# Kernel tuning notes

Hardware: AMD Instinct MI355X
Metric: run time of the kernel (lower is better)

## Reference

```python
import jax, jax.numpy as jnp
import numpy as np

N_MEL = 80; ARNN = 1024; ADIM = 128; EMB = 512; PRE = 256; DRNN = 1024; NF = 32; KS = 31
B = 32; NCTX = 512; T = 500
PAD = (KS - 1) // 2


def setup_inputs() -> dict:
    key = jax.random.key(0)
    ks = jax.random.split(key, 20)
    g = lambda k, shape: jax.random.normal(k, shape, dtype=jnp.float32) * 0.02
    return {
        "memory": jax.random.normal(ks[0], (B, NCTX, EMB), dtype=jnp.float32),
        "decoder_inputs": jax.random.normal(ks[1], (B, N_MEL, T), dtype=jnp.float32),
        "mask": jnp.zeros((B, NCTX), dtype=bool),
        "prenet_w1": g(ks[2], (PRE, N_MEL)),
        "prenet_w2": g(ks[3], (PRE, PRE)),
        "arnn_wih": g(ks[4], (4 * ARNN, PRE + EMB)),
        "arnn_whh": g(ks[5], (4 * ARNN, ARNN)),
        "arnn_bih": jnp.zeros((4 * ARNN,), jnp.float32),
        "arnn_bhh": jnp.zeros((4 * ARNN,), jnp.float32),
        "q_w": g(ks[6], (ADIM, ARNN)),
        "m_w": g(ks[7], (ADIM, EMB)),
        "loc_conv_w": g(ks[8], (NF, 2, KS)),
        "loc_w": g(ks[9], (ADIM, NF)),
        "v_w": g(ks[10], (ADIM,)),
        "drnn_wih": g(ks[11], (4 * DRNN, ARNN + EMB)),
        "drnn_whh": g(ks[12], (4 * DRNN, DRNN)),
        "drnn_bih": jnp.zeros((4 * DRNN,), jnp.float32),
        "drnn_bhh": jnp.zeros((4 * DRNN,), jnp.float32),
        "proj_w": g(ks[13], (N_MEL, DRNN + EMB)),
        "proj_b": jnp.zeros((N_MEL,), jnp.float32),
        "gate_w": g(ks[14], (1, DRNN + EMB)),
        "gate_b": jnp.zeros((1,), jnp.float32),
    }


def _lstm_cell(x, h, c, wih, whh, bih, bhh):
    # PyTorch LSTMCell gate order: i, f, g, o
    z = x @ wih.T + h @ whh.T + bih + bhh
    i, f, g, o = jnp.split(z, 4, axis=-1)
    c2 = jax.nn.sigmoid(f) * c + jax.nn.sigmoid(i) * jnp.tanh(g)
    h2 = jax.nn.sigmoid(o) * jnp.tanh(c2)
    return h2, c2


def reference(memory, decoder_inputs, mask,
              prenet_w1, prenet_w2,
              arnn_wih, arnn_whh, arnn_bih, arnn_bhh,
              q_w, m_w, loc_conv_w, loc_w, v_w,
              drnn_wih, drnn_whh, drnn_bih, drnn_bhh,
              proj_w, proj_b, gate_w, gate_b):
    b, n_ctx, emb = memory.shape
    n_mel, t_out = decoder_inputs.shape[1], decoder_inputs.shape[2]

    # (time, batch, n_mel) with a leading zero go-frame; PreNet (eval: no dropout)
    x = jnp.transpose(decoder_inputs, (2, 0, 1))
    x = jnp.concatenate([jnp.zeros((1, b, n_mel), x.dtype), x], axis=0)
    h = jax.nn.relu(x @ prenet_w1.T)
    h = jax.nn.relu(h @ prenet_w2.T)  # (T+1, B, PRE)
    inputs = h[:-1]  # T decoder steps

    proc_mem = memory @ m_w.T  # (B, n_ctx, ADIM)

    def step(carry, xin):
        ah, ac, dh, dc, aw, awc, actx = carry
        cell_in = jnp.concatenate([xin, actx], axis=-1)
        ah, ac = _lstm_cell(cell_in, ah, ac, arnn_wih, arnn_whh, arnn_bih, arnn_bhh)
        # location-sensitive attention
        aw_cat = jnp.stack([aw, awc], axis=1)  # (B, 2, n_ctx)
        loc = jax.lax.conv_general_dilated(
            aw_cat, loc_conv_w, window_strides=(1,), padding=[(PAD, PAD)],
            dimension_numbers=("NCH", "OIH", "NCH"))  # (B, NF, n_ctx)
        loc = jnp.transpose(loc, (0, 2, 1)) @ loc_w.T  # (B, n_ctx, ADIM)
        q = (ah @ q_w.T)[:, None, :]  # (B, 1, ADIM)
        e = jnp.tanh(q + proc_mem + loc) @ v_w  # (B, n_ctx)
        e = jnp.where(mask, -1e9, e)
        aw = jax.nn.softmax(e, axis=-1)
        actx = jnp.einsum("bn,bne->be", aw, memory)
        awc = awc + aw
        din = jnp.concatenate([ah, actx], axis=-1)
        dh, dc = _lstm_cell(din, dh, dc, drnn_wih, drnn_whh, drnn_bih, drnn_bhh)
        dhc = jnp.concatenate([dh, actx], axis=-1)
        mel = dhc @ proj_w.T + proj_b  # (B, n_mel)
        gate = dhc @ gate_w.T + gate_b  # (B, 1)
        return (ah, ac, dh, dc, aw, awc, actx), (mel, gate[:, 0])

    z32 = lambda *s: jnp.zeros(s, memory.dtype)
    carry0 = (z32(b, ARNN), z32(b, ARNN), z32(b, DRNN), z32(b, DRNN),
              z32(b, n_ctx), z32(b, n_ctx), z32(b, emb))
    _, (mels, gates) = jax.lax.scan(step, carry0, inputs)
    mel_out = jnp.transpose(mels, (1, 2, 0))   # (B, n_mel, T)
    gate_out = jnp.transpose(gates, (1, 0))    # (B, T)
    return mel_out, gate_out
```

## Files before the change

### kernel.cpp

```cpp
#include <hip/hip_runtime.h>

#define NBLK 256
#define NTHR 512

constexpr int kNMel = 80, kArnn = 1024, kAdim = 128, kEmb = 512, kPre = 256;
constexpr int kNF = 32, kKS = 31, kB = 32, kNctx = 512, kT = 500, kPad = 15;

constexpr int KT_A = 56;
constexpr int KT_D = 80;
constexpr int KT_ALL = KT_A + KT_D;

constexpr int OFF_PREB   = 0;
constexpr int OFF_PROCMB = OFF_PREB + kT * kB * kPre / 2;
constexpr int OFF_QWTB   = OFF_PROCMB + kB * kNctx * kAdim / 2;
constexpr int OFF_LWT    = OFF_QWTB + kAdim * kArnn / 2;
constexpr int OFF_STATE  = OFF_LWT + kAdim * 33;
constexpr int OFF_AHB    = OFF_STATE;
constexpr int OFF_DHB    = OFF_AHB + 2 * kB * kArnn / 2;
constexpr int OFF_DH     = OFF_DHB + 2 * kB * kArnn / 2;
constexpr int OFF_AC     = OFF_DH + 2 * kB * kArnn;
constexpr int OFF_DC     = OFF_AC + kB * kArnn;
constexpr int OFF_ACTX   = OFF_DC + kB * kArnn;
constexpr int OFF_AW     = OFF_ACTX + kB * kEmb;
constexpr int OFF_AWC    = OFF_AW + kB * kNctx;
constexpr int OFF_PAW    = OFF_AWC + kB * kNctx;
constexpr int OFF_NUM    = OFF_PAW + kB * kNctx;
constexpr int OFF_DEN    = OFF_NUM + 2 * kB * kEmb;
constexpr int OFF_END    = OFF_DEN + 2 * kB;
constexpr int STATE_SZ   = OFF_END - OFF_STATE;
constexpr int OFF_BAR    = OFF_END;
constexpr int BAR_LINES  = 266;
constexpr int OFF_PAN    = OFF_BAR + BAR_LINES * 32;
constexpr int PAN_SZ     = NBLK * KT_ALL * 256;
constexpr int OFF_GMB    = OFF_PAN + PAN_SZ;
constexpr int GMB_SZ     = kB * kNctx * kEmb / 2;

typedef __attribute__((ext_vector_type(4))) float fvec4;
typedef __attribute__((ext_vector_type(8))) short bh8_t;
typedef unsigned long long u64;
typedef unsigned short ushortt;

union U64u { u64 u; float2 f2; ushortt s[4]; };

constexpr int AH_O = 0;
constexpr int DH_O = 16384;
constexpr int AX_O = 32768;

union SMem {
  struct { ushortt stage[49152]; } x1;
  struct { float zra[4][2][64][4]; float zrd[4][2][64][4];
           float hb[2][32][4]; } x2;
  struct { float ahb_s[kArnn]; float vw_s[kAdim]; float psum[512]; float q_s[kAdim];
           float aw_s[96]; float awc_s[96]; float cw[kNF * 2 * kKS];
           float loc_s[64 * 33]; float p_s[64]; float lwt[kAdim * 33];
           float dhc[kArnn + kEmb]; float pprj[126];
           ushortt pm[64 * kAdim]; } b;
  struct { float x8[8][80]; float h1[8][256]; } p;
  struct { float mem_s[4][512]; } m;
};

__device__ __forceinline__ float sigf(float x) { return 1.0f / (1.0f + __expf(-x)); }
__device__ __forceinline__ float tanhfast(float x) { return 1.0f - 2.0f / (__expf(2.0f * x) + 1.0f); }

__device__ __forceinline__ ushortt bf16rn(float f) {
  unsigned u = __float_as_uint(f);
  unsigned r = (u + 0x7FFFu + ((u >> 16) & 1u)) >> 16;
  return (ushortt)r;
}
__device__ __forceinline__ float bf2f(ushortt v) {
  return __uint_as_float((unsigned)v << 16);
}

__device__ __forceinline__ u64 ald64(const void* p) {
  return __hip_atomic_load((const u64*)p, __ATOMIC_RELAXED, __HIP_MEMORY_SCOPE_AGENT);
}
__device__ __forceinline__ float alf(const float* p) {
  return __hip_atomic_load(p, __ATOMIC_RELAXED, __HIP_MEMORY_SCOPE_AGENT);
}
__device__ __forceinline__ void asf(float* p, float v) {
  __hip_atomic_store(p, v, __ATOMIC_RELAXED, __HIP_MEMORY_SCOPE_AGENT);
}
__device__ __forceinline__ void as64(void* p, u64 v) {
  __hip_atomic_store((u64*)p, v, __ATOMIC_RELAXED, __HIP_MEMORY_SCOPE_AGENT);
}
__device__ __forceinline__ unsigned alu(const unsigned* p) {
  return __hip_atomic_load(p, __ATOMIC_RELAXED, __HIP_MEMORY_SCOPE_AGENT);
}
__device__ __forceinline__ void asu(unsigned* p, unsigned v) {
  __hip_atomic_store(p, v, __ATOMIC_RELAXED, __HIP_MEMORY_SCOPE_AGENT);
}

__device__ __forceinline__ void gbar_full(unsigned* cnt, unsigned* gen, unsigned& genv) {
  __syncthreads();
  if (threadIdx.x == 0) {
    __threadfence();
    unsigned arrived = __hip_atomic_fetch_add(cnt, 1u, __ATOMIC_ACQ_REL, __HIP_MEMORY_SCOPE_AGENT) + 1u;
    if (arrived == (unsigned)NBLK) {
      __hip_atomic_store(cnt, 0u, __ATOMIC_RELAXED, __HIP_MEMORY_SCOPE_AGENT);
      __hip_atomic_fetch_add(gen, 1u, __ATOMIC_ACQ_REL, __HIP_MEMORY_SCOPE_AGENT);
    } else {
      while (__hip_atomic_load(gen, __ATOMIC_ACQUIRE, __HIP_MEMORY_SCOPE_AGENT) == genv) {
        __builtin_amdgcn_s_sleep(2);
      }
    }
    ++genv;
  }
  __syncthreads();
}

__device__ __forceinline__ void gbar_light(unsigned* bar, unsigned target, int bk, int tid) {
  asm volatile("s_waitcnt vmcnt(0) lgkmcnt(0)" ::: "memory");
  __syncthreads();
  if (bk == 0) {
    if (tid < 64) {
      if (tid == 0) asm volatile("s_waitcnt vmcnt(0)" ::: "memory");
      unsigned i0 = (unsigned)tid * 4, i1 = i0 + 1, i2 = i0 + 2, i3 = i0 + 3;
      for (;;) {
        bool ok = true;
        if (i0 != 0) ok = ok && (alu(&bar[i0 * 32]) >= target);
        ok = ok && (alu(&bar[i1 * 32]) >= target);
        ok = ok && (alu(&bar[i2 * 32]) >= target);
        ok = ok && (alu(&bar[i3 * 32]) >= target);
        if (__all(ok)) break;
        __builtin_amdgcn_s_sleep(1);
      }
      if (tid < 8) asu(&bar[(256 + tid) * 32], target);
    }
  } else {
    if (tid == 0) {
      asm volatile("s_waitcnt vmcnt(0)" ::: "memory");
      asu(&bar[bk * 32], target);
      unsigned* wk = &bar[(256 + (bk & 7)) * 32];
      while (alu(wk) < target) __builtin_amdgcn_s_sleep(1);
    }
  }
  __syncthreads();
}

__device__ __forceinline__ void stage_half1(int tid, const ushortt* __restrict__ AHBq,
    const ushortt* __restrict__ DHBp, const float* __restrict__ numq,
    const float* __restrict__ invden, ushortt* __restrict__ lds)
{
  const int uc = tid & 127;
  const int r0 = tid >> 7;
  const int chunk = uc >> 4, u8c = uc & 15;
  u64 va[8], vd[8], ax[8];
  #pragma unroll
  for (int i = 0; i < 8; ++i) {
    int row = r0 + 4 * i;
    va[i] = ald64(AHBq + (size_t)row * 1024 + uc * 4);
    vd[i] = ald64(DHBp + (size_t)row * 1024 + uc * 4);
  }
  #pragma unroll
  for (int i = 0; i < 8; ++i) {
    int row = r0 + 4 * i;
    const float* np = numq + (size_t)row * 512 + uc * 4;
    U64u a, b; a.u = ald64(np); b.u = ald64(np + 2);
    float s = invden[row];
    U64u pk;
    pk.s[0] = bf16rn(a.f2.x * s);  pk.s[1] = bf16rn(a.f2.y * s);
    pk.s[2] = bf16rn(b.f2.x * s);  pk.s[3] = bf16rn(b.f2.y * s);
    ax[i] = pk.u;
  }
  #pragma unroll
  for (int i = 0; i < 8; ++i) {
    int row = r0 + 4 * i;
    int sw = u8c ^ ((row & 7) << 1);
    int off = chunk * 2048 + row * 64 + sw * 4;
    *reinterpret_cast<u64*>(lds + AH_O + off) = va[i];
    *reinterpret_cast<u64*>(lds + DH_O + off) = vd[i];
    *reinterpret_cast<u64*>(lds + AX_O + off) = ax[i];
  }
}
__device__ __forceinline__ void load_half2(int tid, const ushortt* __restrict__ AHBq,
    const ushortt* __restrict__ DHBp, u64* va, u64* vd)
{
  const int uc = tid & 127, r0 = tid >> 7;
  #pragma unroll
  for (int i = 0; i < 8; ++i) {
    int row = r0 + 4 * i;
    va[i] = ald64(AHBq + (size_t)row * 1024 + 512 + uc * 4);
    vd[i] = ald64(DHBp + (size_t)row * 1024 + 512 + uc * 4);
  }
}
__device__ __forceinline__ void write_half2(int tid, const u64* va, const u64* vd,
                                            ushortt* __restrict__ lds)
{
  const int uc = tid & 127, r0 = tid >> 7;
  const int chunk = uc >> 4, u8c = uc & 15;
  #pragma unroll
  for (int i = 0; i < 8; ++i) {
    int row = r0 + 4 * i;
    int sw = u8c ^ ((row & 7) << 1);
    int off = chunk * 2048 + row * 64 + sw * 4;
    *reinterpret_cast<u64*>(lds + AH_O + off) = va[i];
    *reinterpret_cast<u64*>(lds + DH_O + off) = vd[i];
  }
}

__device__ constexpr int lds_base(int LS, int kt) {
  if (LS == 0) {
    if (kt < 24) return AX_O + ((kt - 8) >> 1) * 2048;
    if (kt < 40) return AH_O + ((kt - 24) >> 1) * 2048;
    return AH_O + ((kt - 40) >> 1) * 2048;
  } else {
    if (kt < 16) return AH_O + (kt >> 1) * 2048;
    if (kt < 32) return AH_O + ((kt - 16) >> 1) * 2048;
    if (kt < 48) return AX_O + ((kt - 32) >> 1) * 2048;
    if (kt < 64) return DH_O + ((kt - 48) >> 1) * 2048;
    return DH_O + ((kt - 64) >> 1) * 2048;
  }
}

template<int LS, int W, int HALF>
__device__ __forceinline__ void consume(const ushortt* __restrict__ lds,
    const short* __restrict__ pan, const ushortt* __restrict__ preb_t,
    int l, fvec4& z0, fvec4& z1)
{
  const int m = l & 15, kg = l >> 4;
  bh8_t fA[4], fB[4], fC[4];
  auto ld4 = [&](int kt0, bh8_t* f) {
    #pragma unroll
    for (int i = 0; i < 4; ++i)
      f[i] = *reinterpret_cast<const bh8_t*>(pan + (size_t)(kt0 + i) * 512 + l * 8);
  };
  auto run4 = [&](int kt0, bh8_t* f) {
    #pragma unroll
    for (int i = 0; i < 4; ++i) {
      const int kt = kt0 + i;
      const int base = lds_base(LS, kt);
      const int sw = (2 * ((kt & 1) * 4 + kg)) ^ ((m & 7) << 1);
      bh8_t a0 = *reinterpret_cast<const bh8_t*>(lds + base + m * 64 + sw * 4);
      bh8_t a1 = *reinterpret_cast<const bh8_t*>(lds + base + (16 + m) * 64 + sw * 4);
      z0 = __builtin_amdgcn_mfma_f32_16x16x32_bf16(a0, f[i], z0, 0, 0, 0);
      z1 = __builtin_amdgcn_mfma_f32_16x16x32_bf16(a1, f[i], z1, 0, 0, 0);
    }
  };
  if constexpr (LS == 0 && HALF == 0) {
    ld4(8 + 4 * W, fA); ld4(24 + 4 * W, fB);
    run4(8 + 4 * W, fA); run4(24 + 4 * W, fB);
  } else if constexpr (LS == 0 && HALF == 1) {
    bh8_t p0[2], p1[2], pf[2];
    #pragma unroll
    for (int i = 0; i < 2; ++i) {
      const int kt = 2 * W + i;
      p0[i] = *reinterpret_cast<const bh8_t*>(preb_t + (size_t)m * 256 + kt * 32 + kg * 8);
      p1[i] = *reinterpret_cast<const bh8_t*>(preb_t + (size_t)(16 + m) * 256 + kt * 32 + kg * 8);
      pf[i] = *reinterpret_cast<const bh8_t*>(pan + (size_t)kt * 512 + l * 8);
    }
    ld4(40 + 4 * W, fA);
    #pragma unroll
    for (int i = 0; i < 2; ++i) {
      z0 = __builtin_amdgcn_mfma_f32_16x16x32_bf16(p0[i], pf[i], z0, 0, 0, 0);
      z1 = __builtin_amdgcn_mfma_f32_16x16x32_bf16(p1[i], pf[i], z1, 0, 0, 0);
    }
    run4(40 + 4 * W, fA);
  } else if constexpr (LS == 1 && HALF == 0) {
    ld4(4 * W, fA); ld4(32 + 4 * W, fB); ld4(48 + 4 * W, fC);
    run4(4 * W, fA); run4(32 + 4 * W, fB); run4(48 + 4 * W, fC);
  } else {
    ld4(16 + 4 * W, fA); ld4(64 + 4 * W, fB);
    run4(16 + 4 * W, fA); run4(64 + 4 * W, fB);
  }
}

extern "C" __global__ void __launch_bounds__(NTHR, 1)
decoder_kernel(const float* __restrict__ gmem, const float* __restrict__ dec,
               const unsigned char* __restrict__ mask,
               const float* __restrict__ pw1, const float* __restrict__ pw2,
               const float* __restrict__ awih, const float* __restrict__ awhh,
               const float* __restrict__ abih, const float* __restrict__ abhh,
               const float* __restrict__ qw, const float* __restrict__ mw,
               const float* __restrict__ cvw, const float* __restrict__ locw,
               const float* __restrict__ vw,
               const float* __restrict__ dwih, const float* __restrict__ dwhh,
               const float* __restrict__ dbih, const float* __restrict__ dbhh,
               const float* __restrict__ pjw, const float* __restrict__ pjb,
               const float* __restrict__ gw, const float* __restrict__ gb,
               float* __restrict__ out, float* __restrict__ ws, int useg)
{
  __shared__ SMem sm;
  __shared__ float s_invden[32];
  const int bk = blockIdx.x, tid = threadIdx.x;
  unsigned genv_f = 0, bcnt = 0;
  unsigned* bar = reinterpret_cast<unsigned*>(ws + OFF_BAR);
  unsigned* cntF = &bar[264 * 32];
  unsigned* genF = &bar[265 * 32];

  ushortt* PREBu = reinterpret_cast<ushortt*>(ws + OFF_PREB);
  ushortt* PROCMBu = reinterpret_cast<ushortt*>(ws + OFF_PROCMB);
  ushortt* QWTBu = reinterpret_cast<ushortt*>(ws + OFF_QWTB);
  float* LWT = ws + OFF_LWT;
  ushortt* AHBu = reinterpret_cast<ushortt*>(ws + OFF_AHB);
  ushortt* DHBu = reinterpret_cast<ushortt*>(ws + OFF_DHB);
  float* DH = ws + OFF_DH;
  float* AC = ws + OFF_AC;
  float* DC = ws + OFF_DC;
  float* ACTX = ws + OFF_ACTX;
  float* AWp = ws + OFF_AW;
  float* AWC = ws + OFF_AWC;
  float* PAW = ws + OFF_PAW;
  float* NUM = ws + OFF_NUM;
  float* DEN = ws + OFF_DEN;
  short* PANS = reinterpret_cast<short*>(ws + OFF_PAN);
  ushortt* GMB = reinterpret_cast<ushortt*>(ws + OFF_GMB);

  for (int i = bk * NTHR + tid; i < STATE_SZ; i += NBLK * NTHR) (ws + OFF_STATE)[i] = 0.f;
  for (int i = bk * NTHR + tid; i < kAdim * kArnn; i += NBLK * NTHR)
    QWTBu[i] = bf16rn(qw[i]);
  for (int i = bk * NTHR + tid; i < kAdim * kNF; i += NBLK * NTHR) {
    int d = i >> 5, f = i & 31;
    LWT[d * 33 + f] = locw[i];
  }
  gbar_full(cntF, genF, genv_f);

  if (bk == 0 && tid < 2 * kB) asf(&DEN[tid], 1.0f);
  for (int it = 0; it < 16; ++it) {
    int task0 = bk * 64 + it * 4;
    for (int i = tid; i < 2048; i += NTHR) {
      int pr = i >> 9, h = i & 511;
      sm.m.mem_s[pr][h] = gmem[(size_t)(task0 + pr) * kEmb + h];
    }
    __syncthreads();
    {
      int pr = tid >> 7, d = tid & 127;
      const float* mwr = mw + d * kEmb;
      float acc = 0.f;
      for (int h = 0; h < kEmb; ++h) acc = fmaf(sm.m.mem_s[pr][h], mwr[h], acc);
      PROCMBu[(size_t)(task0 + pr) * kAdim + d] = bf16rn(acc);
    }
    if (useg) {
      for (int i = tid; i < 2048; i += NTHR) {
        int pr = i >> 9, h = i & 511;
        GMB[(size_t)(task0 + pr) * kEmb + h] = bf16rn(sm.m.mem_s[pr][h]);
      }
    }
    __syncthreads();
  }
  for (int g = bk; g < 2000; g += NBLK) {
    int t_idx = g >> 2;
    int b0 = (g & 3) * 8;
    if (t_idx == 0) {
      for (int i = tid; i < 8 * kPre; i += NTHR)
        PREBu[(size_t)(b0 + (i >> 8)) * kPre + (i & 255)] = 0;
      continue;
    }
    for (int i = tid; i < 640; i += NTHR) {
      int bb = i / 80, m2 = i % 80;
      sm.p.x8[bb][m2] = dec[((size_t)(b0 + bb) * kNMel + m2) * kT + (t_idx - 1)];
    }
    __syncthreads();
    {
      int u = tid & 255, rep = tid >> 8;
      float acc[4] = {0.f, 0.f, 0.f, 0.f};
      for (int m2 = 0; m2 < 80; ++m2) {
        float w = pw1[u * kNMel + m2];
        #pragma unroll
        for (int r = 0; r < 4; ++r) acc[r] = fmaf(w, sm.p.x8[rep * 4 + r][m2], acc[r]);
      }
      #pragma unroll
      for (int r = 0; r < 4; ++r) sm.p.h1[rep * 4 + r][u] = fmaxf(acc[r], 0.f);
    }
    __syncthreads();
    {
      int u = tid & 255, rep = tid >> 8;
      float acc[4] = {0.f, 0.f, 0.f, 0.f};
      for (int k = 0; k < kPre; ++k) {
        float w = pw2[u * kPre + k];
        #pragma unroll
        for (int r = 0; r < 4; ++r) acc[r] = fmaf(w, sm.p.h1[rep * 4 + r][k], acc[r]);
      }
      #pragma unroll
      for (int r = 0; r < 4; ++r)
        PREBu[((size_t)t_idx * kB + b0 + rep * 4 + r) * kPre + u] = bf16rn(fmaxf(acc[r], 0.f));
    }
    __syncthreads();
  }
  {
    const int UNITS = NBLK * KT_ALL * 64;
    for (int u = bk * NTHR + tid; u < UNITS; u += NBLK * NTHR) {
      int bkk = u / (KT_ALL * 64);
      int rem = u - bkk * (KT_ALL * 64);
      int kta = rem >> 6, l = rem & 63;
      int lstm = (kta >= KT_A);
      int kt = lstm ? kta - KT_A : kta;
      int n = l & 15, kg = l >> 4;
      int r = (n >> 2) * 1024 + bkk * 4 + (n & 3);
      bh8_t v;
      #pragma unroll
      for (int j = 0; j < 8; ++j) {
        int k = kt * 32 + kg * 8 + j;
        float wv;
        if (!lstm) wv = (k < 768) ? awih[(size_t)r * 768 + k] : awhh[(size_t)r * 1024 + (k - 768)];
        else       wv = (k < 1536) ? dwih[(size_t)r * 1536 + k] : dwhh[(size_t)r * 1024 + (k - 1536)];
        v[j] = (short)bf16rn(wv);
      }
      *reinterpret_cast<bh8_t*>(PANS + (size_t)u * 8) = v;
    }
  }
  gbar_full(cntF, genF, genv_f);

  for (int t = 0; t <= kT; ++t) {
    const int p = t & 1, q = p ^ 1;
    float* nump = NUM + p * kB * kEmb;
    const float* numq = NUM + q * kB * kEmb;
    const ushortt* AHBq_ = AHBu + q * kB * kArnn;
    const ushortt* DHBp_ = DHBu + p * kB * kArnn;

    if (tid < kB) s_invden[tid] = 1.0f / alf(DEN + q * kB + tid);
    __syncthreads();
    if (t > 0 && tid < 64) {
      int idx = bk * 64 + tid;
      int b2 = idx >> 9;
      float invd = s_invden[b2];
      float av = PAW[idx] * invd;
      asf(&AWp[idx], av);
      asf(&AWC[idx], alf(&AWC[idx]) + av);
      asf(&ACTX[idx], alf(&numq[idx]) * invd);
    }
    if (t < kT) {
      if (tid < 64) asf(&nump[bk * 64 + tid], 0.f);
      if (bk == 0 && tid < kB) asf(DEN + p * kB + tid, 0.f);
    }
    {
      ushortt* XL = reinterpret_cast<ushortt*>(&sm);
      stage_half1(tid, AHBq_, DHBp_, numq, s_invden, XL);
      u64 vA2[8], vD2[8];
      load_half2(tid, AHBq_, DHBp_, vA2, vD2);
      __syncthreads();
      const int w8 = tid >> 6, l = tid & 63;
      fvec4 z0 = {0.f, 0.f, 0.f, 0.f}, z1 = z0;
      const ushortt* preb_t = PREBu + (size_t)t * kB * kPre;
      const short* panb = PANS + (size_t)bk * (KT_ALL * 512);
      const short* pand = panb + KT_A * 512;
      const bool aA = (w8 < 4) && (t < kT);
      const bool aD = (w8 >= 4) && (t > 0);
      if (aA) {
        switch (w8) {
          case 0: consume<0, 0, 0>(XL, panb, preb_t, l, z0, z1); break;
          case 1: consume<0, 1, 0>(XL, panb, preb_t, l, z0, z1); break;
          case 2: consume<0, 2, 0>(XL, panb, preb_t, l, z0, z1); break;
          default: consume<0, 3, 0>(XL, panb, preb_t, l, z0, z1); break;
        }
      } else if (aD) {
        switch (w8) {
          case 4: consume<1, 0, 0>(XL, pand, preb_t, l, z0, z1); break;
          case 5: consume<1, 1, 0>(XL, pand, preb_t, l, z0, z1); break;
          case 6: consume<1, 2, 0>(XL, pand, preb_t, l, z0, z1); break;
          default: consume<1, 3, 0>(XL, pand, preb_t, l, z0, z1); break;
        }
      }
      __syncthreads();
      write_half2(tid, vA2, vD2, XL);
      __syncthreads();
      if (aA) {
        switch (w8) {
          case 0: consume<0, 0, 1>(XL, panb, preb_t, l, z0, z1); break;
          case 1: consume<0, 1, 1>(XL, panb, preb_t, l, z0, z1); break;
          case 2: consume<0, 2, 1>(XL, panb, preb_t, l, z0, z1); break;
          default: consume<0, 3, 1>(XL, panb, preb_t, l, z0, z1); break;
        }
      } else if (aD) {
        switch (w8) {
          case 4: consume<1, 0, 1>(XL, pand, preb_t, l, z0, z1); break;
          case 5: consume<1, 1, 1>(XL, pand, preb_t, l, z0, z1); break;
          case 6: consume<1, 2, 1>(XL, pand, preb_t, l, z0, z1); break;
          default: consume<1, 3, 1>(XL, pand, preb_t, l, z0, z1); break;
        }
      }
      __syncthreads();
      if (w8 < 4) {
        *reinterpret_cast<fvec4*>(&sm.x2.zra[w8][0][l][0]) = z0;
        *reinterpret_cast<fvec4*>(&sm.x2.zra[w8][1][l][0]) = z1;
      } else {
        *reinterpret_cast<fvec4*>(&sm.x2.zrd[w8 - 4][0][l][0]) = z0;
        *reinterpret_cast<fvec4*>(&sm.x2.zrd[w8 - 4][1][l][0]) = z1;
      }
    }
    __syncthreads();
    if (tid < 256) {
      const int ls = tid >> 7, uu = (tid >> 5) & 3, b = tid & 31;
      const bool go = (ls == 0) ? (t < kT) : (t > 0);
      if (go) {
        const int mt = b >> 4, mm = b & 15;
        const int lane_base = (mm >> 2) * 16, rr = mm & 3;
        float zg[4];
        #pragma unroll
        for (int g = 0; g < 4; ++g) {
          int ln = lane_base + g * 4 + uu;
          float s;
          if (ls == 0)
            s = sm.x2.zra[0][mt][ln][rr] + sm.x2.zra[1][mt][ln][rr]
              + sm.x2.zra[2][mt][ln][rr] + sm.x2.zra[3][mt][ln][rr];
          else
            s = sm.x2.zrd[0][mt][ln][rr] + sm.x2.zrd[1][mt][ln][rr]
              + sm.x2.zrd[2][mt][ln][rr] + sm.x2.zrd[3][mt][ln][rr];
          int rg = g * 1024 + bk * 4 + uu;
          s += (ls ? dbih[rg] + dbhh[rg] : abih[rg] + abhh[rg]);
          zg[g] = s;
        }
        float* cst = ls ? DC : AC;
        const int idx = b * kArnn + bk * 4 + uu;
        float c = sigf(zg[1]) * cst[idx] + sigf(zg[0]) * tanhfast(zg[2]);
        cst[idx] = c;
        float h = sigf(zg[3]) * tanhfast(c);
        if (ls) asf(&DH[q * kB * kArnn + idx], h);
        sm.x2.hb[ls][b][uu] = h;
      }
    }
    __syncthreads();
    if (tid < 64) {
      int ls = tid >> 5, b = tid & 31;
      bool go2 = ls ? (t > 0) : (t < kT);
      if (go2) {
        U64u pk;
        #pragma unroll
        for (int j = 0; j < 4; ++j) pk.s[j] = bf16rn(sm.x2.hb[ls][b][j]);
        ushortt* dst = (ls ? (DHBu + q * kB * kArnn) : (AHBu + p * kB * kArnn)) + b * kArnn + bk * 4;
        as64(dst, pk.u);
      }
    }
    gbar_light(bar, ++bcnt, bk, tid);

    if (t < kT) {
      const int b = bk >> 3, sub = bk & 7, j0 = sub * 64;
      const int pbase = (sub == 0) ? 0 : 21 + (sub - 1) * 20;
      const int pcnt = (sub == 0) ? 21 : 20;
      const ushortt* AHBp_ = AHBu + p * kB * kArnn;
      if (tid < 256) {
        U64u v; v.u = ald64(AHBp_ + b * kArnn + tid * 4);
        #pragma unroll
        for (int j = 0; j < 4; ++j) sm.b.ahb_s[tid * 4 + j] = bf2f(v.s[j]);
      }
      for (int i = tid; i < 94; i += NTHR) {
        int jj = j0 - kPad + i;
        bool ok = (jj >= 0 && jj < kNctx);
        sm.b.aw_s[i] = ok ? alf(&AWp[b * kNctx + jj]) : 0.f;
        sm.b.awc_s[i] = ok ? alf(&AWC[b * kNctx + jj]) : 0.f;
      }
      for (int i = tid; i < kNF * 2 * kKS; i += NTHR) sm.b.cw[i] = cvw[i];
      for (int i = tid; i < kAdim * 33; i += NTHR) sm.b.lwt[i] = LWT[i];
      for (int i = tid; i < kAdim; i += NTHR) sm.b.vw_s[i] = vw[i];
      {
        const fvec4* src = reinterpret_cast<const fvec4*>(PROCMBu + (size_t)(b * kNctx + j0) * kAdim);
        fvec4* dst = reinterpret_cast<fvec4*>(sm.b.pm);
        for (int i = tid; i < 1024; i += NTHR) dst[i] = src[i];
      }
      if (sub < 4 && t > 0) {
        for (int i = tid; i < kArnn + kEmb; i += NTHR)
          sm.b.dhc[i] = (i < kArnn) ? alf(&DH[q * kB * kArnn + b * kArnn + i])
                                    : alf(&ACTX[b * kEmb + (i - kArnn)]);
      }
      __syncthreads();
      {
        int d = tid & 127, qr = tid >> 7;
        const ushortt* wq = QWTBu + (size_t)d * kArnn + qr * 256;
        const float* ahs = sm.b.ahb_s + qr * 256;
        float acc = 0.f;
        #pragma unroll 4
        for (int h8 = 0; h8 < 32; ++h8) {
          U64u a, c2;
          a.u = *reinterpret_cast<const u64*>(wq + h8 * 8);
          c2.u = *reinterpret_cast<const u64*>(wq + h8 * 8 + 4);
          #pragma unroll
          for (int j = 0; j < 4; ++j) acc = fmaf(bf2f(a.s[j]), ahs[h8 * 8 + j], acc);
          #pragma unroll
          for (int j = 0; j < 4; ++j) acc = fmaf(bf2f(c2.s[j]), ahs[h8 * 8 + 4 + j], acc);
        }
        sm.b.psum[tid] = acc;
      }
      __syncthreads();
      if (tid < kAdim)
        sm.b.q_s[tid] = sm.b.psum[tid] + sm.b.psum[128 + tid]
                      + sm.b.psum[256 + tid] + sm.b.psum[384 + tid];
      {
        int j = tid >> 3, f0 = (tid & 7) * 4;
        #pragma unroll
        for (int fi = 0; fi < 4; ++fi) {
          int f = f0 + fi;
          const float* w0 = &sm.b.cw[f * 62];
          float s = 0.f;
          for (int k = 0; k < kKS; ++k)
            s = fmaf(sm.b.aw_s[j + k], w0[k], fmaf(sm.b.awc_s[j + k], w0[31 + k], s));
          sm.b.loc_s[j * 33 + f] = s;
        }
      }
      if (sub < 4 && t > 0 && tid < pcnt * 6) {
        int ol = tid / 6, kc = tid % 6, og = pbase + ol;
        const float* row = (og < kNMel) ? pjw + (size_t)og * (kArnn + kEmb) : gw;
        const float* x = sm.b.dhc + kc * 256;
        const float* r2 = row + kc * 256;
        float acc = 0.f;
        for (int k = 0; k < 256; ++k) acc = fmaf(r2[k], x[k], acc);
        sm.b.pprj[tid] = acc;
      }
      __syncthreads();
      {
        int j = tid >> 3, grp = tid & 7, jj = j0 + j;
        float pe = 0.f;
        #pragma unroll 4
        for (int dd = 0; dd < 16; ++dd) {
          int d = grp + 8 * dd;
          float l2 = 0.f;
          const float* ls2 = &sm.b.loc_s[j * 33];
          const float* lw2 = &sm.b.lwt[d * 33];
          #pragma unroll 8
          for (int f = 0; f < kNF; ++f) l2 = fmaf(ls2[f], lw2[f], l2);
          float x = sm.b.q_s[d] + bf2f(sm.b.pm[j * kAdim + d]) + l2;
          pe = fmaf(sm.b.vw_s[d], tanhfast(x), pe);
        }
        pe += __shfl_xor(pe, 1);
        pe += __shfl_xor(pe, 2);
        pe += __shfl_xor(pe, 4);
        if (grp == 0) {
          float pv = mask[b * kNctx + jj] ? 0.f : __expf(pe);
          sm.b.p_s[j] = pv;
          PAW[b * kNctx + jj] = pv;
        }
      }
      if (sub < 4 && t > 0 && tid < pcnt) {
        int og = pbase + tid;
        float val = (og < kNMel) ? pjb[og] : gb[0];
        #pragma unroll
        for (int kc = 0; kc < 6; ++kc) val += sm.b.pprj[tid * 6 + kc];
        if (og < kNMel) out[((size_t)b * kNMel + og) * kT + (t - 1)] = val;
        else out[(size_t)kB * kNMel * kT + b * kT + (t - 1)] = val;
      }
      __syncthreads();
      if (tid < 64) {
        float v = sm.b.p_s[tid];
        #pragma unroll
        for (int o = 1; o < 64; o <<= 1) v += __shfl_xor(v, o);
        if (tid == 0) atomicAdd(DEN + p * kB + b, v);
      }
      if (useg) {
        const ushortt* memb = GMB + (size_t)(b * kNctx + j0) * kEmb + tid;
        float a0 = 0.f, a1 = 0.f, a2 = 0.f, a3 = 0.f;
        #pragma unroll 4
        for (int jj2 = 0; jj2 < 64; jj2 += 4) {
          a0 = fmaf(sm.b.p_s[jj2],     bf2f(memb[(size_t)jj2 * kEmb]), a0);
          a1 = fmaf(sm.b.p_s[jj2 + 1], bf2f(memb[(size_t)(jj2 + 1) * kEmb]), a1);
          a2 = fmaf(sm.b.p_s[jj2 + 2], bf2f(memb[(size_t)(jj2 + 2) * kEmb]), a2);
          a3 = fmaf(sm.b.p_s[jj2 + 3], bf2f(memb[(size_t)(jj2 + 3) * kEmb]), a3);
        }
        atomicAdd(&nump[b * kEmb + tid], (a0 + a1) + (a2 + a3));
      } else {
        const float* memb = gmem + (size_t)(b * kNctx + j0) * kEmb + tid;
        float a0 = 0.f, a1 = 0.f;
        #pragma unroll 8
        for (int jj2 = 0; jj2 < 64; jj2 += 2) {
          a0 = fmaf(sm.b.p_s[jj2], memb[(size_t)jj2 * kEmb], a0);
          a1 = fmaf(sm.b.p_s[jj2 + 1], memb[(size_t)(jj2 + 1) * kEmb], a1);
        }
        atomicAdd(&nump[b * kEmb + tid], a0 + a1);
      }
      gbar_light(bar, ++bcnt, bk, tid);
    }
  }

  if (bk < kB) {
    const int b = bk;
    for (int i = tid; i < kArnn + kEmb; i += NTHR)
      sm.b.dhc[i] = (i < kArnn) ? alf(&DH[1 * kB * kArnn + b * kArnn + i])
                                : alf(&ACTX[b * kEmb + (i - kArnn)]);
    __syncthreads();
    if (tid < 486) {
      int ol = tid / 6, kc = tid % 6;
      const float* row = (ol < kNMel) ? pjw + (size_t)ol * (kArnn + kEmb) : gw;
      const float* x = sm.b.dhc + kc * 256;
      const float* r2 = row + kc * 256;
      float acc = 0.f;
      for (int k = 0; k < 256; ++k) acc = fmaf(r2[k], x[k], acc);
      sm.b.psum[tid] = acc;
    }
    __syncthreads();
    if (tid < 81) {
      float val = (tid < kNMel) ? pjb[tid] : gb[0];
      #pragma unroll
      for (int kc = 0; kc < 6; ++kc) val += sm.b.psum[tid * 6 + kc];
      if (tid < kNMel) out[((size_t)b * kNMel + tid) * kT + (kT - 1)] = val;
      else out[(size_t)kB * kNMel * kT + b * kT + (kT - 1)] = val;
    }
  }
}

extern "C" void kernel_launch(void* const* d_in, const int* in_sizes, int n_in,
                              void* d_out, int out_size, void* d_ws, size_t ws_size,
                              hipStream_t stream) {
  const float* gmem = (const float*)d_in[0];
  const float* dec = (const float*)d_in[1];
  const unsigned char* mask = (const unsigned char*)d_in[2];
  const float* pw1 = (const float*)d_in[3];
  const float* pw2 = (const float*)d_in[4];
  const float* awih = (const float*)d_in[5];
  const float* awhh = (const float*)d_in[6];
  const float* abih = (const float*)d_in[7];
  const float* abhh = (const float*)d_in[8];
  const float* qw = (const float*)d_in[9];
  const float* mw = (const float*)d_in[10];
  const float* cvw = (const float*)d_in[11];
  const float* locw = (const float*)d_in[12];
  const float* vw = (const float*)d_in[13];
  const float* dwih = (const float*)d_in[14];
  const float* dwhh = (const float*)d_in[15];
  const float* dbih = (const float*)d_in[16];
  const float* dbhh = (const float*)d_in[17];
  const float* pjw = (const float*)d_in[18];
  const float* pjb = (const float*)d_in[19];
  const float* gw = (const float*)d_in[20];
  const float* gb = (const float*)d_in[21];
  float* out = (float*)d_out;
  float* ws = (float*)d_ws;

  int useg = (ws_size >= (size_t)(OFF_GMB + GMB_SZ) * sizeof(float)) ? 1 : 0;

  hipMemsetAsync((char*)d_ws + (size_t)OFF_BAR * sizeof(float), 0,
                 (size_t)BAR_LINES * 128, stream);
  hipLaunchKernelGGL(decoder_kernel, dim3(NBLK), dim3(NTHR), 0, stream,
                     gmem, dec, mask, pw1, pw2, awih, awhh, abih, abhh, qw, mw,
                     cvw, locw, vw, dwih, dwhh, dbih, dbhh, pjw, pjb, gw, gb,
                     out, ws, useg);
}
```

Baseline: 39.91 ms.

## Concentrate LSTM gate GEMMs on 64 blocks with per-wave full-K tiles

The LSTM gate matmuls were split over all 256 blocks, each handling 4 hidden units, with the K dimension split across waves and reduced through LDS. Now only 64 blocks do the LSTM work, each owning 16 hidden units. Each wave computes a full-K 16x16 tile for both LSTMs and does its own gate math, so the cross-wave partial-sum reduction goes away. The remaining 192 blocks sit idle during this phase. Each active block streams four times as many weight panels per step, which puts the LSTM phase's global load bandwidth on fewer CUs.

```diff
diff --git a/kernel.cpp b/kernel.cpp
--- a/kernel.cpp
+++ b/kernel.cpp
@@ -2,6 +2,7 @@
 
 #define NBLK 256
 #define NTHR 512
+#define NLB 64
 
 constexpr int kNMel = 80, kArnn = 1024, kAdim = 128, kEmb = 512, kPre = 256;
 constexpr int kNF = 32, kKS = 31, kB = 32, kNctx = 512, kT = 500, kPad = 15;
@@ -31,7 +32,7 @@
 constexpr int OFF_BAR    = OFF_END;
 constexpr int BAR_LINES  = 266;
 constexpr int OFF_PAN    = OFF_BAR + BAR_LINES * 32;
-constexpr int PAN_SZ     = NBLK * KT_ALL * 256;
+constexpr int PAN_SZ     = NLB * 4 * KT_ALL * 256;
 constexpr int OFF_GMB    = OFF_PAN + PAN_SZ;
 constexpr int GMB_SZ     = kB * kNctx * kEmb / 2;
 
@@ -47,9 +48,9 @@
 constexpr int AX_O = 32768;
 
 union SMem {
-  struct { ushortt stage[49152]; } x1;
-  struct { float zra[4][2][64][4]; float zrd[4][2][64][4];
-           float hb[2][32][4]; } x2;
+  struct { ushortt stage[49152];
+           float zs[8][2][64][4];
+           float hb[2][32][16]; } x1;
   struct { float ahb_s[kArnn]; float vw_s[kAdim]; float psum[512]; float q_s[kAdim];
            float aw_s[96]; float awc_s[96]; float cw[kNF * 2 * kKS];
            float loc_s[64 * 33]; float p_s[64]; float lwt[kAdim * 33];
@@ -212,55 +213,27 @@
   }
 }
 
-template<int LS, int W, int HALF>
-__device__ __forceinline__ void consume(const ushortt* __restrict__ lds,
-    const short* __restrict__ pan, const ushortt* __restrict__ preb_t,
-    int l, fvec4& z0, fvec4& z1)
+template<int LS, int HALF>
+__device__ __forceinline__ void lstm_half(const ushortt* __restrict__ lds,
+    const short* __restrict__ panw, const ushortt* __restrict__ preb_t,
+    int row, int m, int kg, int l, fvec4& z)
 {
-  const int m = l & 15, kg = l >> 4;
-  bh8_t fA[4], fB[4], fC[4];
-  auto ld4 = [&](int kt0, bh8_t* f) {
-    #pragma unroll
-    for (int i = 0; i < 4; ++i)
-      f[i] = *reinterpret_cast<const bh8_t*>(pan + (size_t)(kt0 + i) * 512 + l * 8);
-  };
-  auto run4 = [&](int kt0, bh8_t* f) {
-    #pragma unroll
-    for (int i = 0; i < 4; ++i) {
-      const int kt = kt0 + i;
+  constexpr int N = (LS == 0) ? (HALF == 0 ? 32 : 24) : (HALF == 0 ? 48 : 32);
+  #pragma unroll
+  for (int i = 0; i < N; ++i) {
+    int kt;
+    if (LS == 0) kt = (HALF == 0) ? (8 + i) : (i < 8 ? i : 32 + i);
+    else         kt = (HALF == 0) ? (i < 16 ? i : i + 16) : (i < 16 ? 16 + i : 48 + i);
+    bh8_t f = *reinterpret_cast<const bh8_t*>(panw + (size_t)((LS ? KT_A : 0) + kt) * 512 + l * 8);
+    bh8_t a;
+    if (LS == 0 && kt < 8) {
+      a = *reinterpret_cast<const bh8_t*>(preb_t + (size_t)row * kPre + kt * 32 + kg * 8);
+    } else {
       const int base = lds_base(LS, kt);
       const int sw = (2 * ((kt & 1) * 4 + kg)) ^ ((m & 7) << 1);
-      bh8_t a0 = *reinterpret_cast<const bh8_t*>(lds + base + m * 64 + sw * 4);
-      bh8_t a1 = *reinterpret_cast<const bh8_t*>(lds + base + (16 + m) * 64 + sw * 4);
-      z0 = __builtin_amdgcn_mfma_f32_16x16x32_bf16(a0, f[i], z0, 0, 0, 0);
-      z1 = __builtin_amdgcn_mfma_f32_16x16x32_bf16(a1, f[i], z1, 0, 0, 0);
-    }
-  };
-  if constexpr (LS == 0 && HALF == 0) {
-    ld4(8 + 4 * W, fA); ld4(24 + 4 * W, fB);
-    run4(8 + 4 * W, fA); run4(24 + 4 * W, fB);
-  } else if constexpr (LS == 0 && HALF == 1) {
-    bh8_t p0[2], p1[2], pf[2];
-    #pragma unroll
-    for (int i = 0; i < 2; ++i) {
-      const int kt = 2 * W + i;
-      p0[i] = *reinterpret_cast<const bh8_t*>(preb_t + (size_t)m * 256 + kt * 32 + kg * 8);
-      p1[i] = *reinterpret_cast<const bh8_t*>(preb_t + (size_t)(16 + m) * 256 + kt * 32 + kg * 8);
-      pf[i] = *reinterpret_cast<const bh8_t*>(pan + (size_t)kt * 512 + l * 8);
-    }
-    ld4(40 + 4 * W, fA);
-    #pragma unroll
-    for (int i = 0; i < 2; ++i) {
-      z0 = __builtin_amdgcn_mfma_f32_16x16x32_bf16(p0[i], pf[i], z0, 0, 0, 0);
-      z1 = __builtin_amdgcn_mfma_f32_16x16x32_bf16(p1[i], pf[i], z1, 0, 0, 0);
-    }
-    run4(40 + 4 * W, fA);
-  } else if constexpr (LS == 1 && HALF == 0) {
-    ld4(4 * W, fA); ld4(32 + 4 * W, fB); ld4(48 + 4 * W, fC);
-    run4(4 * W, fA); run4(32 + 4 * W, fB); run4(48 + 4 * W, fC);
-  } else {
-    ld4(16 + 4 * W, fA); ld4(64 + 4 * W, fB);
-    run4(16 + 4 * W, fA); run4(64 + 4 * W, fB);
+      a = *reinterpret_cast<const bh8_t*>(lds + base + row * 64 + sw * 4);
+    }
+    z = __builtin_amdgcn_mfma_f32_16x16x32_bf16(a, f, z, 0, 0, 0);
   }
 }
 
@@ -377,15 +350,17 @@
     __syncthreads();
   }
   {
-    const int UNITS = NBLK * KT_ALL * 64;
+    const int UNITS = NLB * 4 * KT_ALL * 64;
     for (int u = bk * NTHR + tid; u < UNITS; u += NBLK * NTHR) {
-      int bkk = u / (KT_ALL * 64);
-      int rem = u - bkk * (KT_ALL * 64);
+      int lb = u / (4 * KT_ALL * 64);
+      int rem = u - lb * (4 * KT_ALL * 64);
+      int nt = rem / (KT_ALL * 64);
+      rem -= nt * (KT_ALL * 64);
       int kta = rem >> 6, l = rem & 63;
       int lstm = (kta >= KT_A);
       int kt = lstm ? kta - KT_A : kta;
       int n = l & 15, kg = l >> 4;
-      int r = (n >> 2) * 1024 + bkk * 4 + (n & 3);
+      int r = (n >> 2) * 1024 + lb * 16 + nt * 4 + (n & 3);
       bh8_t v;
       #pragma unroll
       for (int j = 0; j < 8; ++j) {
@@ -422,102 +397,71 @@
       if (tid < 64) asf(&nump[bk * 64 + tid], 0.f);
       if (bk == 0 && tid < kB) asf(DEN + p * kB + tid, 0.f);
     }
-    {
+    if (bk < NLB) {
       ushortt* XL = reinterpret_cast<ushortt*>(&sm);
       stage_half1(tid, AHBq_, DHBp_, numq, s_invden, XL);
       u64 vA2[8], vD2[8];
       load_half2(tid, AHBq_, DHBp_, vA2, vD2);
       __syncthreads();
       const int w8 = tid >> 6, l = tid & 63;
-      fvec4 z0 = {0.f, 0.f, 0.f, 0.f}, z1 = z0;
+      const int nt = w8 & 3, mh = w8 >> 2;
+      const int m = l & 15, kg = l >> 4, row = mh * 16 + m;
+      fvec4 za = {0.f, 0.f, 0.f, 0.f}, zd = za;
       const ushortt* preb_t = PREBu + (size_t)t * kB * kPre;
-      const short* panb = PANS + (size_t)bk * (KT_ALL * 512);
-      const short* pand = panb + KT_A * 512;
-      const bool aA = (w8 < 4) && (t < kT);
-      const bool aD = (w8 >= 4) && (t > 0);
-      if (aA) {
-        switch (w8) {
-          case 0: consume<0, 0, 0>(XL, panb, preb_t, l, z0, z1); break;
-          case 1: consume<0, 1, 0>(XL, panb, preb_t, l, z0, z1); break;
-          case 2: consume<0, 2, 0>(XL, panb, preb_t, l, z0, z1); break;
-          default: consume<0, 3, 0>(XL, panb, preb_t, l, z0, z1); break;
-        }
-      } else if (aD) {
-        switch (w8) {
-          case 4: consume<1, 0, 0>(XL, pand, preb_t, l, z0, z1); break;
-          case 5: consume<1, 1, 0>(XL, pand, preb_t, l, z0, z1); break;
-          case 6: consume<1, 2, 0>(XL, pand, preb_t, l, z0, z1); break;
-          default: consume<1, 3, 0>(XL, pand, preb_t, l, z0, z1); break;
-        }
-      }
+      const short* panw = PANS + (size_t)(bk * 4 + nt) * KT_ALL * 512;
+      if (t < kT) lstm_half<0, 0>(XL, panw, preb_t, row, m, kg, l, za);
+      if (t > 0)  lstm_half<1, 0>(XL, panw, preb_t, row, m, kg, l, zd);
       __syncthreads();
       write_half2(tid, vA2, vD2, XL);
       __syncthreads();
-      if (aA) {
-        switch (w8) {
-          case 0: consume<0, 0, 1>(XL, panb, preb_t, l, z0, z1); break;
-          case 1: consume<0, 1, 1>(XL, panb, preb_t, l, z0, z1); break;
-          case 2: consume<0, 2, 1>(XL, panb, preb_t, l, z0, z1); break;
-          default: consume<0, 3, 1>(XL, panb, preb_t, l, z0, z1); break;
-        }
-      } else if (aD) {
-        switch (w8) {
-          case 4: consume<1, 0, 1>(XL, pand, preb_t, l, z0, z1); break;
-          case 5: consume<1, 1, 1>(XL, pand, preb_t, l, z0, z1); break;
-          case 6: consume<1, 2, 1>(XL, pand, preb_t, l, z0, z1); break;
-          default: consume<1, 3, 1>(XL, pand, preb_t, l, z0, z1); break;
-        }
-      }
-      __syncthreads();
-      if (w8 < 4) {
-        *reinterpret_cast<fvec4*>(&sm.x2.zra[w8][0][l][0]) = z0;
-        *reinterpret_cast<fvec4*>(&sm.x2.zra[w8][1][l][0]) = z1;
-      } else {
-        *reinterpret_cast<fvec4*>(&sm.x2.zrd[w8 - 4][0][l][0]) = z0;
-        *reinterpret_cast<fvec4*>(&sm.x2.zrd[w8 - 4][1][l][0]) = z1;
-      }
-    }
-    __syncthreads();
-    if (tid < 256) {
-      const int ls = tid >> 7, uu = (tid >> 5) & 3, b = tid & 31;
-      const bool go = (ls == 0) ? (t < kT) : (t > 0);
-      if (go) {
-        const int mt = b >> 4, mm = b & 15;
-        const int lane_base = (mm >> 2) * 16, rr = mm & 3;
-        float zg[4];
-        #pragma unroll
-        for (int g = 0; g < 4; ++g) {
-          int ln = lane_base + g * 4 + uu;
-          float s;
-          if (ls == 0)
-            s = sm.x2.zra[0][mt][ln][rr] + sm.x2.zra[1][mt][ln][rr]
-              + sm.x2.zra[2][mt][ln][rr] + sm.x2.zra[3][mt][ln][rr];
-          else
-            s = sm.x2.zrd[0][mt][ln][rr] + sm.x2.zrd[1][mt][ln][rr]
-              + sm.x2.zrd[2][mt][ln][rr] + sm.x2.zrd[3][mt][ln][rr];
-          int rg = g * 1024 + bk * 4 + uu;
-          s += (ls ? dbih[rg] + dbhh[rg] : abih[rg] + abhh[rg]);
-          zg[g] = s;
-        }
-        float* cst = ls ? DC : AC;
-        const int idx = b * kArnn + bk * 4 + uu;
-        float c = sigf(zg[1]) * cst[idx] + sigf(zg[0]) * tanhfast(zg[2]);
-        cst[idx] = c;
-        float h = sigf(zg[3]) * tanhfast(c);
-        if (ls) asf(&DH[q * kB * kArnn + idx], h);
-        sm.x2.hb[ls][b][uu] = h;
-      }
-    }
-    __syncthreads();
-    if (tid < 64) {
-      int ls = tid >> 5, b = tid & 31;
-      bool go2 = ls ? (t > 0) : (t < kT);
-      if (go2) {
-        U64u pk;
-        #pragma unroll
-        for (int j = 0; j < 4; ++j) pk.s[j] = bf16rn(sm.x2.hb[ls][b][j]);
-        ushortt* dst = (ls ? (DHBu + q * kB * kArnn) : (AHBu + p * kB * kArnn)) + b * kArnn + bk * 4;
-        as64(dst, pk.u);
+      if (t < kT) lstm_half<0, 1>(XL, panw, preb_t, row, m, kg, l, za);
+      if (t > 0)  lstm_half<1, 1>(XL, panw, preb_t, row, m, kg, l, zd);
+      __syncthreads();
+      *reinterpret_cast<fvec4*>(&sm.x1.zs[w8][0][l][0]) = za;
+      *reinterpret_cast<fvec4*>(&sm.x1.zs[w8][1][l][0]) = zd;
+      __syncthreads();
+      {
+        const int u4 = l & 3, bi = l >> 2, b = mh * 16 + bi;
+        const int col = bk * 16 + nt * 4 + u4;
+        const int lsrc = (bi >> 2) * 16, jsrc = bi & 3;
+        const int idx = b * kArnn + col;
+        if (t < kT) {
+          float zg[4];
+          #pragma unroll
+          for (int g = 0; g < 4; ++g) {
+            int rg = g * 1024 + col;
+            zg[g] = sm.x1.zs[w8][0][lsrc + g * 4 + u4][jsrc] + abih[rg] + abhh[rg];
+          }
+          float c = sigf(zg[1]) * AC[idx] + sigf(zg[0]) * tanhfast(zg[2]);
+          AC[idx] = c;
+          sm.x1.hb[0][b][nt * 4 + u4] = sigf(zg[3]) * tanhfast(c);
+        }
+        if (t > 0) {
+          float zg[4];
+          #pragma unroll
+          for (int g = 0; g < 4; ++g) {
+            int rg = g * 1024 + col;
+            zg[g] = sm.x1.zs[w8][1][lsrc + g * 4 + u4][jsrc] + dbih[rg] + dbhh[rg];
+          }
+          float c = sigf(zg[1]) * DC[idx] + sigf(zg[0]) * tanhfast(zg[2]);
+          DC[idx] = c;
+          float h = sigf(zg[3]) * tanhfast(c);
+          sm.x1.hb[1][b][nt * 4 + u4] = h;
+          asf(&DH[q * kB * kArnn + idx], h);
+        }
+      }
+      __syncthreads();
+      if (tid < 256) {
+        int ls = tid >> 7, rem = tid & 127, b = rem >> 2, q4 = rem & 3;
+        bool go2 = ls ? (t > 0) : (t < kT);
+        if (go2) {
+          U64u pk;
+          #pragma unroll
+          for (int j = 0; j < 4; ++j) pk.s[j] = bf16rn(sm.x1.hb[ls][b][q4 * 4 + j]);
+          ushortt* dst = (ls ? (DHBu + q * kB * kArnn) : (AHBu + p * kB * kArnn))
+                         + b * kArnn + bk * 16 + q4 * 4;
+          as64(dst, pk.u);
+        }
       }
     }
     gbar_light(bar, ++bcnt, bk, tid);
```

Result: slower. 59.78 ms (+49.8%).
